# Performance work log

Measured on AMD Instinct MI355X. Metric: run time of the kernel, lower is better.

## Reference

```python
import jax, jax.numpy as jnp
import numpy as np
from jax import lax

REG_STRENGTH = 0.01
TEMPERATURE = 0.1


def _pav_nonincreasing(y):
    """Pool-adjacent-violators for isotonic L2 regression with a
    nonincreasing constraint (matches torchsort's isotonic_l2).
    Returns (solution [n], block_id [n])."""
    n = y.shape[0]

    def body(carry, yi):
        m, c, t = carry  # block means, block counts, stack top
        m = m.at[t].set(yi)
        c = c.at[t].set(1)

        def cond(st):
            m_, c_, t_ = st
            return (t_ > 0) & (m_[t_ - 1] < m_[t_])

        def merge(st):
            m_, c_, t_ = st
            tot = m_[t_ - 1] * c_[t_ - 1] + m_[t_] * c_[t_]
            cc = c_[t_ - 1] + c_[t_]
            m_ = m_.at[t_ - 1].set(tot / cc)
            c_ = c_.at[t_ - 1].set(cc).at[t_].set(0)
            return (m_, c_, t_ - 1)

        m, c, t = lax.while_loop(cond, merge, (m, c, t))
        return (m, c, t + 1), None

    init = (jnp.zeros(n, y.dtype), jnp.zeros(n, jnp.int32), jnp.int32(0))
    (m, c, _), _ = lax.scan(body, init, y)
    sol = jnp.repeat(m, c, total_repeat_length=n)
    blk = jnp.repeat(jnp.arange(n), c, total_repeat_length=n)
    return sol, blk


@jax.custom_vjp
def _isotonic_l2(y):
    return _pav_nonincreasing(y)[0]


def _iso_fwd(y):
    sol, blk = _pav_nonincreasing(y)
    return sol, blk


def _iso_bwd(blk, g):
    n = g.shape[0]
    sums = jax.ops.segment_sum(g, blk, num_segments=n)
    cnts = jax.ops.segment_sum(jnp.ones_like(g), blk, num_segments=n)
    return ((sums / jnp.maximum(cnts, 1.0))[blk],)


_isotonic_l2.defvjp(_iso_fwd, _iso_bwd)


def soft_sort_ascending(scores, reg_strength):
    """torchsort.soft_sort with L2 regularization. scores: [B, R]."""
    n = scores.shape[-1]
    w = jnp.arange(n, 0, -1, dtype=scores.dtype) / reg_strength  # [n, ..., 1]/rs
    perm = jnp.argsort(scores, axis=-1)
    s = -jnp.take_along_axis(scores, perm, axis=-1)  # descending sort of -scores
    sol = jax.vmap(_isotonic_l2)(w[None, :] - s)
    return sol - w  # ascending soft-sorted values, [B, R]


def setup_inputs() -> dict:
    key = jax.random.key(0)
    k1, k2 = jax.random.split(key)
    scores = jax.random.normal(k1, (128, 8192), dtype=jnp.float32)
    ref_class = jax.random.randint(k2, (8192,), 0, 10, dtype=jnp.int32)
    return {"scores": scores, "ref_class": ref_class, "k": 32, "K": 8}


def reference(scores, ref_class, k, K):
    B, R = scores.shape
    rc = ref_class
    if rc.ndim == 1:
        rc = jnp.broadcast_to(rc[None, :], (B, R))
    rc = rc.astype(scores.dtype)
    sorted_vals = soft_sort_ascending(scores, REG_STRENGTH)  # [B, R]
    yk = sorted_vals[:, -k:]                                  # top-k largest, [B, k]
    M = jnp.abs(scores[:, None, :] - yk[:, :, None])          # [B, k, R]
    soft_mask = jax.nn.softmax(-M / TEMPERATURE, axis=-1)     # [B, k, R]
    soft_label_expectation = jnp.einsum('bkr,br->bk', soft_mask, rc)
    return yk, soft_label_expectation
```

## Files before the change

### kernel.cpp

```cpp
#include <hip/hip_runtime.h>
#include <math.h>

#define R_N   8192
#define K_TOP 32
#define TPB   1024
#define NEG_INVT_LOG2E (-14.426950408889634f)

__device__ __forceinline__ float fast_exp2(float x) {
#if __has_builtin(__builtin_amdgcn_exp2f)
    return __builtin_amdgcn_exp2f(x);
#else
    return exp2f(x);
#endif
}

__device__ __forceinline__ float sort32_asc(float v, int l) {
#pragma unroll
    for (int k = 2; k <= 32; k <<= 1) {
#pragma unroll
        for (int j = k >> 1; j > 0; j >>= 1) {
            float pv = __shfl_xor(v, j, 64);
            bool up = ((l & k) == 0);
            bool lower = ((l & j) == 0);
            v = (lower == up) ? fminf(v, pv) : fmaxf(v, pv);
        }
    }
    return v;
}

__device__ __forceinline__ float merge_asc32(float v, int l) {
#pragma unroll
    for (int j = 16; j > 0; j >>= 1) {
        float pv = __shfl_xor(v, j, 64);
        v = ((l & j) == 0) ? fminf(v, pv) : fmaxf(v, pv);
    }
    return v;
}

extern "C" __global__ void __launch_bounds__(TPB)
sast_fused(const float* __restrict__ scores, const int* __restrict__ rc,
           float* __restrict__ out, int B) {
    __shared__ float sdata[R_N];
    __shared__ unsigned char cdata[R_N];
    __shared__ float topbuf[32 * 32];
    __shared__ float yk_lds[K_TOP];

    const int row = blockIdx.x;
    const int tid = threadIdx.x;
    const int l   = tid & 31;
    const int h   = tid >> 5;

    const float4* s4 = (const float4*)(scores + (size_t)row * R_N);
    const int4*   c4 = (const int4*)rc;
    float v[8];
#pragma unroll
    for (int q = 0; q < 2; ++q) {
        int idx4 = tid + q * TPB;
        float4 s = s4[idx4];
        int4   c = c4[idx4];
        int r = idx4 * 4;
        sdata[r + 0] = s.x; sdata[r + 1] = s.y;
        sdata[r + 2] = s.z; sdata[r + 3] = s.w;
        ((unsigned int*)cdata)[idx4] =
            (unsigned int)(c.x & 0xff) | ((unsigned int)(c.y & 0xff) << 8) |
            ((unsigned int)(c.z & 0xff) << 16) | ((unsigned int)(c.w & 0xff) << 24);
        v[q * 4 + 0] = s.x; v[q * 4 + 1] = s.y;
        v[q * 4 + 2] = s.z; v[q * 4 + 3] = s.w;
    }

    float run = sort32_asc(v[0], l);
#pragma unroll
    for (int p = 1; p < 8; ++p) {
        float sv  = sort32_asc(v[p], l);
        float rev = __shfl_xor(sv, 31, 64);
        run = fmaxf(run, rev);
        run = merge_asc32(run, l);
    }

#pragma unroll
    for (int stride = 1; stride < 32; stride <<= 1) {
        topbuf[h * 32 + l] = run;
        __syncthreads();
        if ((h & (2 * stride - 1)) == 0) {
            float pv = topbuf[(h + stride) * 32 + (l ^ 31)];
            run = fmaxf(run, pv);
            run = merge_asc32(run, l);
        }
        __syncthreads();
    }

    if (tid < 32) {
        yk_lds[l] = run;
        out[(size_t)row * K_TOP + l] = run;
    }
    __syncthreads();

    const int   j = h;
    const float y = yk_lds[j];
    float num = 0.0f, den = 0.0f;
#pragma unroll 8
    for (int i = 0; i < R_N / 32; ++i) {
        int r   = i * 32 + l;
        float s = sdata[r];
        float c = (float)cdata[r];
        float e = fast_exp2(NEG_INVT_LOG2E * fabsf(s - y));
        num = fmaf(e, c, num);
        den += e;
    }
#pragma unroll
    for (int off = 16; off > 0; off >>= 1) {
        num += __shfl_xor(num, off, 64);
        den += __shfl_xor(den, off, 64);
    }
    if (l == 0) {
        out[(size_t)B * K_TOP + (size_t)row * K_TOP + j] = num / den;
    }
}

extern "C" void kernel_launch(void* const* d_in, const int* in_sizes, int n_in,
                              void* d_out, int out_size, void* d_ws, size_t ws_size,
                              hipStream_t stream) {
    const float* scores = (const float*)d_in[0];
    const int*   rc     = (const int*)d_in[1];
    const int R = in_sizes[1];
    const int B = in_sizes[0] / R;
    float* out = (float*)d_out;
    hipLaunchKernelGGL(sast_fused, dim3(B), dim3(TPB), 0, stream, scores, rc, out, B);
}
```

Baseline: 80.58 us.

## Split fused kernel into top-k, sliced expectation, and final reduction kernels

The single per-row kernel becomes three launches. A top-k kernel uses a tree merge of per-thread sorted lists in place of a serial chain. An expectation kernel splits each row into 8 slices across 1024 blocks of 256 threads, with interleaved float2 score/class pairs in LDS. A final kernel sums the partials and divides. This lifts parallelism above 128 blocks on a many-CU GPU, at the cost of extra launches, a second read of scores and a workspace round trip.

```diff
diff --git a/kernel.cpp b/kernel.cpp
--- a/kernel.cpp
+++ b/kernel.cpp
@@ -1,10 +1,11 @@
 #include <hip/hip_runtime.h>
 #include <math.h>
 
-#define R_N   8192
-#define K_TOP 32
-#define TPB   1024
-#define NEG_INVT_LOG2E (-14.426950408889634f)
+#define R_N    8192
+#define K_TOP  32
+#define NSLICE 8
+#define SLICE  (R_N / NSLICE)
+#define NEG10_LOG2E (-14.426950408889634f)
 
 __device__ __forceinline__ float fast_exp2(float x) {
 #if __has_builtin(__builtin_amdgcn_exp2f)
@@ -14,19 +15,6 @@
 #endif
 }
 
-__device__ __forceinline__ float sort32_asc(float v, int l) {
-#pragma unroll
-    for (int k = 2; k <= 32; k <<= 1) {
-#pragma unroll
-        for (int j = k >> 1; j > 0; j >>= 1) {
-            float pv = __shfl_xor(v, j, 64);
-            bool up = ((l & k) == 0);
-            bool lower = ((l & j) == 0);
-            v = (lower == up) ? fminf(v, pv) : fmaxf(v, pv);
-        }
-    }
-    return v;
-}
 
 __device__ __forceinline__ float merge_asc32(float v, int l) {
 #pragma unroll
@@ -37,45 +25,45 @@
     return v;
 }
 
-extern "C" __global__ void __launch_bounds__(TPB)
-sast_fused(const float* __restrict__ scores, const int* __restrict__ rc,
-           float* __restrict__ out, int B) {
-    __shared__ float sdata[R_N];
-    __shared__ unsigned char cdata[R_N];
+__device__ __forceinline__ float sort32_asc(float v, int l) {
+#pragma unroll
+    for (int k = 2; k <= 32; k <<= 1) {
+#pragma unroll
+        for (int j = k >> 1; j > 0; j >>= 1) {
+            float pv = __shfl_xor(v, j, 64);
+            bool keep_min = (((l & k) == 0) == ((l & j) == 0));
+            v = keep_min ? fminf(v, pv) : fmaxf(v, pv);
+        }
+    }
+    return v;
+}
+
+__device__ __forceinline__ float merge_top32(float a, float b, int l) {
+    float rev = __shfl_xor(b, 31, 64);
+    return merge_asc32(fmaxf(a, rev), l);
+}
+
+extern "C" __global__ void __launch_bounds__(1024)
+k_topk(const float* __restrict__ scores, float* __restrict__ out) {
     __shared__ float topbuf[32 * 32];
-    __shared__ float yk_lds[K_TOP];
-
     const int row = blockIdx.x;
     const int tid = threadIdx.x;
     const int l   = tid & 31;
     const int h   = tid >> 5;
 
     const float4* s4 = (const float4*)(scores + (size_t)row * R_N);
-    const int4*   c4 = (const int4*)rc;
-    float v[8];
+    float4 a = s4[tid];
+    float4 b = s4[tid + 1024];
+    float v[8] = {a.x, a.y, a.z, a.w, b.x, b.y, b.z, b.w};
+
 #pragma unroll
-    for (int q = 0; q < 2; ++q) {
-        int idx4 = tid + q * TPB;
-        float4 s = s4[idx4];
-        int4   c = c4[idx4];
-        int r = idx4 * 4;
-        sdata[r + 0] = s.x; sdata[r + 1] = s.y;
-        sdata[r + 2] = s.z; sdata[r + 3] = s.w;
-        ((unsigned int*)cdata)[idx4] =
-            (unsigned int)(c.x & 0xff) | ((unsigned int)(c.y & 0xff) << 8) |
-            ((unsigned int)(c.z & 0xff) << 16) | ((unsigned int)(c.w & 0xff) << 24);
-        v[q * 4 + 0] = s.x; v[q * 4 + 1] = s.y;
-        v[q * 4 + 2] = s.z; v[q * 4 + 3] = s.w;
-    }
-
-    float run = sort32_asc(v[0], l);
+    for (int p = 0; p < 8; ++p) v[p] = sort32_asc(v[p], l);
 #pragma unroll
-    for (int p = 1; p < 8; ++p) {
-        float sv  = sort32_asc(v[p], l);
-        float rev = __shfl_xor(sv, 31, 64);
-        run = fmaxf(run, rev);
-        run = merge_asc32(run, l);
-    }
+    for (int gap = 1; gap < 8; gap <<= 1)
+#pragma unroll
+        for (int p = 0; p < 8; p += 2 * gap)
+            v[p] = merge_top32(v[p], v[p + gap], l);
+    float run = v[0];
 
 #pragma unroll
     for (int stride = 1; stride < 32; stride <<= 1) {
@@ -83,38 +71,73 @@
         __syncthreads();
         if ((h & (2 * stride - 1)) == 0) {
             float pv = topbuf[(h + stride) * 32 + (l ^ 31)];
-            run = fmaxf(run, pv);
-            run = merge_asc32(run, l);
+            run = merge_asc32(fmaxf(run, pv), l);
         }
         __syncthreads();
     }
+    if (tid < 32) out[(size_t)row * K_TOP + l] = run;
+}
 
-    if (tid < 32) {
-        yk_lds[l] = run;
-        out[(size_t)row * K_TOP + l] = run;
-    }
+extern "C" __global__ void __launch_bounds__(256)
+k_expect(const float* __restrict__ scores, const int* __restrict__ rc,
+         const float* __restrict__ yk, float* __restrict__ part) {
+    __shared__ float2 sc[SLICE];
+    __shared__ float  yk_lds[K_TOP];
+    __shared__ float  rnum[4][K_TOP], rden[4][K_TOP];
+
+    const int row = blockIdx.x >> 3;
+    const int sl  = blockIdx.x & (NSLICE - 1);
+    const int tid = threadIdx.x;
+    const int j   = tid & 31;
+    const int t   = tid >> 5;
+
+    const float4* s4 = (const float4*)(scores + (size_t)row * R_N + sl * SLICE);
+    const int4*   c4 = (const int4*)(rc + sl * SLICE);
+    float4 s = s4[tid];
+    int4   c = c4[tid];
+    float4* scv = (float4*)sc;
+    scv[tid * 2 + 0] = make_float4(s.x, (float)c.x, s.y, (float)c.y);
+    scv[tid * 2 + 1] = make_float4(s.z, (float)c.z, s.w, (float)c.w);
+    if (tid < K_TOP) yk_lds[tid] = yk[(size_t)row * K_TOP + tid];
     __syncthreads();
 
-    const int   j = h;
     const float y = yk_lds[j];
     float num = 0.0f, den = 0.0f;
+    const float2* base = &sc[t * (SLICE / 8)];
 #pragma unroll 8
-    for (int i = 0; i < R_N / 32; ++i) {
-        int r   = i * 32 + l;
-        float s = sdata[r];
-        float c = (float)cdata[r];
-        float e = fast_exp2(NEG_INVT_LOG2E * fabsf(s - y));
-        num = fmaf(e, c, num);
+    for (int i = 0; i < SLICE / 8; ++i) {
+        float2 p = base[i];
+        float e = fast_exp2(NEG10_LOG2E * fabsf(p.x - y));
+        num = fmaf(e, p.y, num);
         den += e;
     }
+    num += __shfl_xor(num, 32, 64);
+    den += __shfl_xor(den, 32, 64);
+    const int wv = tid >> 6;
+    if ((tid & 63) < 32) { rnum[wv][j] = num; rden[wv][j] = den; }
+    __syncthreads();
+    if (tid < K_TOP) {
+        float n2 = rnum[0][tid] + rnum[1][tid] + rnum[2][tid] + rnum[3][tid];
+        float d2 = rden[0][tid] + rden[1][tid] + rden[2][tid] + rden[3][tid];
+        float* dst = part + ((size_t)row * NSLICE + sl) * (2 * K_TOP);
+        dst[tid] = n2;
+        dst[K_TOP + tid] = d2;
+    }
+}
+
+extern "C" __global__ void __launch_bounds__(256)
+k_final(const float* __restrict__ part, float* __restrict__ out, int B) {
+    const int g   = blockIdx.x * 256 + threadIdx.x;
+    const int row = g >> 5;
+    const int j   = g & 31;
+    const float* p = part + (size_t)row * NSLICE * (2 * K_TOP);
+    float num = 0.0f, den = 0.0f;
 #pragma unroll
-    for (int off = 16; off > 0; off >>= 1) {
-        num += __shfl_xor(num, off, 64);
-        den += __shfl_xor(den, off, 64);
+    for (int s = 0; s < NSLICE; ++s) {
+        num += p[s * 2 * K_TOP + j];
+        den += p[s * 2 * K_TOP + K_TOP + j];
     }
-    if (l == 0) {
-        out[(size_t)B * K_TOP + (size_t)row * K_TOP + j] = num / den;
-    }
+    out[(size_t)B * K_TOP + g] = num / den;
 }
 
 extern "C" void kernel_launch(void* const* d_in, const int* in_sizes, int n_in,
@@ -124,6 +147,10 @@
     const int*   rc     = (const int*)d_in[1];
     const int R = in_sizes[1];
     const int B = in_sizes[0] / R;
-    float* out = (float*)d_out;
-    hipLaunchKernelGGL(sast_fused, dim3(B), dim3(TPB), 0, stream, scores, rc, out, B);
+    float* out  = (float*)d_out;
+    float* part = (float*)d_ws;
+
+    hipLaunchKernelGGL(k_topk,   dim3(B),           dim3(1024), 0, stream, scores, out);
+    hipLaunchKernelGGL(k_expect, dim3(B * NSLICE),  dim3(256),  0, stream, scores, rc, out, part);
+    hipLaunchKernelGGL(k_final,  dim3((B * K_TOP) / 256), dim3(256), 0, stream, part, out, B);
 }
```

Result: faster. 77.91 us (-3.3%).
